# Optimization experiments

Measured on AMD Instinct MI355X. Metric: run time of the kernel, lower is better.

## Reference

```python
import jax, jax.numpy as jnp
import numpy as np

B, D, C = 4096, 256, 32000
T = 1.0
P_MARGIN = 0.5
N_MARGIN = 0.5
W_BU = 1.0
W_MS = 0.0
SIM_CAP = 0.999999


def setup_inputs() -> dict:
    key = jax.random.key(0)
    k1, k2, k3, k4, k5 = jax.random.split(key, 5)
    inputs = jax.random.normal(k1, (B, D), dtype=jnp.float32)
    inputs = inputs / jnp.linalg.norm(inputs, axis=1, keepdims=True)  # re-id features are L2-normalized
    targets = jax.random.randint(k2, (B,), 0, C, dtype=jnp.int32)
    indexs = jnp.arange(B, dtype=jnp.int32)
    label_to_pairs = jax.random.randint(k3, (B, 2), 0, B, dtype=jnp.int32)
    all_label_to_clusterid = jax.random.randint(k4, (C,), 0, C, dtype=jnp.int32)
    V = jax.random.normal(k5, (C, D), dtype=jnp.float32)
    V = V / jnp.linalg.norm(V, axis=1, keepdims=True)  # memory bank rows kept unit-norm by EMA update
    return {"inputs": inputs, "targets": targets, "indexs": indexs,
            "label_to_pairs": label_to_pairs,
            "all_label_to_clusterid": all_label_to_clusterid, "V": V}


def _ms_loss(inputs, targets):
    # vectorized form of ExLoss.ms with ms_table=False:
    # psims[i] = sims[i, targets==targets[i]], nsims[i] = sims[i, targets!=targets[i]]
    sims = inputs @ inputs.T  # [B, B]
    pos = targets[:, None] == targets[None, :]
    neg = ~pos
    NEG_BIG = jnp.float32(-1e30)
    POS_BIG = jnp.float32(1e30)
    p_thrd = jnp.where(neg.any(axis=1),
                       jnp.where(neg, sims, NEG_BIG).max(axis=1),
                       jnp.float32(-3.0)) + P_MARGIN
    n_thrd = jnp.where(pos.any(axis=1),
                       jnp.where(pos, sims, POS_BIG).min(axis=1),
                       jnp.float32(3.0)) - N_MARGIN
    hp = pos & (sims < p_thrd[:, None])
    hn = neg & (sims > n_thrd[:, None]) & (sims < SIM_CAP)
    hp_cnt = hp.sum()
    hn_cnt = hn.sum()
    # BCE-with-logits: target 1 -> softplus(-x); target 0 -> softplus(x); mean over kept elems
    hp_loss = jnp.where(hp_cnt > 0,
                        jnp.where(hp, jax.nn.softplus(-sims), 0.0).sum()
                        / jnp.maximum(hp_cnt, 1).astype(sims.dtype),
                        jnp.float32(0.0))
    hn_loss = jnp.where(hn_cnt > 0,
                        jnp.where(hn, jax.nn.softplus(sims), 0.0).sum()
                        / jnp.maximum(hn_cnt, 1).astype(sims.dtype),
                        jnp.float32(0.0))
    return hp_loss + hn_loss


def reference(inputs, targets, indexs, label_to_pairs, all_label_to_clusterid, V):
    # Exclusive.forward: logits against the memory bank
    tsims = inputs @ V.T            # [B, C]
    outputs = tsims * T
    # bu cross-entropy (weight=None, mean reduction)
    logp = jax.nn.log_softmax(outputs, axis=-1)
    bu_loss = -jnp.take_along_axis(logp, targets[:, None].astype(jnp.int32), axis=1).mean()
    ms_loss = _ms_loss(inputs, targets)
    loss = W_MS * ms_loss + W_BU * bu_loss
    return (loss, outputs)
```

## Files before the change

kernel.cpp:

```cpp
#include <hip/hip_runtime.h>
#include <hip/hip_bf16.h>
#include <stdint.h>

#define NB 4096
#define ND 256
#define NC 32000
#define NCT (NC / 128)

typedef __bf16 bf16x8 __attribute__((ext_vector_type(8)));
typedef float  f32x4  __attribute__((ext_vector_type(4)));

__device__ __forceinline__ unsigned short f32_to_bf16(float f) {
  union { float f; uint32_t u; } v; v.f = f;
  uint32_t r = v.u + 0x7fffu + ((v.u >> 16) & 1u);
  return (unsigned short)(r >> 16);
}

__global__ void prep_kernel(const float* __restrict__ inA,
                            const float* __restrict__ inV,
                            unsigned short* __restrict__ outA,
                            unsigned short* __restrict__ outV,
                            float* __restrict__ loss) {
  int gid = blockIdx.x * blockDim.x + threadIdx.x;
  int stride = gridDim.x * blockDim.x;
  if (gid == 0) *loss = 0.f;
  const int nA4 = NB * ND / 4;
  const int nV4 = NC * ND / 4;
  for (int i = gid; i < nA4 + nV4; i += stride) {
    float4 v = (i < nA4) ? ((const float4*)inA)[i]
                         : ((const float4*)inV)[i - nA4];
    ushort4 o;
    o.x = f32_to_bf16(v.x);
    o.y = f32_to_bf16(v.y);
    o.z = f32_to_bf16(v.z);
    o.w = f32_to_bf16(v.w);
    if (i < nA4) ((ushort4*)outA)[i] = o;
    else         ((ushort4*)outV)[i - nA4] = o;
  }
}

__global__ void __launch_bounds__(256, 2)
gemm_expsum_kernel(const unsigned short* __restrict__ A,
                   const unsigned short* __restrict__ V,
                   float* __restrict__ out,
                   float* __restrict__ partial) {
  __shared__ float red[2][128];

  const int b = blockIdx.x;
  const int xcd = b & 7;
  const int s = b >> 3;
  const int colt = (xcd << 5) + (s & 31);
  const int rowt = s >> 5;
  if (colt >= NCT) return;
  const int brow = rowt << 7;
  const int bcol = colt << 7;

  const int tid  = threadIdx.x;
  const int lane = tid & 63;
  const int wave = tid >> 6;
  const int wr   = wave >> 1;
  const int wc   = wave & 1;
  const int c16  = lane & 15;
  const int kq   = lane >> 4;

  const __bf16* Ab = (const __bf16*)A;
  const __bf16* Vb = (const __bf16*)V;
  const __bf16* aBase = Ab + (size_t)(brow + wr * 64 + c16) * ND + kq * 8;
  const __bf16* bBase = Vb + (size_t)(bcol + wc * 64 + c16) * ND + kq * 8;

  f32x4 acc[4][4];
#pragma unroll
  for (int c = 0; c < 4; ++c)
#pragma unroll
    for (int r = 0; r < 4; ++r)
      acc[c][r] = (f32x4){0.f, 0.f, 0.f, 0.f};

  bf16x8 a0[4], b0[4], a1[4], b1[4];

#define LOADF(AF, BF, KT)                                                     \
  do {                                                                        \
    _Pragma("unroll")                                                         \
    for (int m = 0; m < 4; ++m)                                               \
      AF[m] = *(const bf16x8*)(aBase + (size_t)m * 16 * ND + (KT) * 32);      \
    _Pragma("unroll")                                                         \
    for (int n = 0; n < 4; ++n)                                               \
      BF[n] = *(const bf16x8*)(bBase + (size_t)n * 16 * ND + (KT) * 32);      \
  } while (0)

#define MFMAALL(AF, BF)                                                       \
  do {                                                                        \
    _Pragma("unroll")                                                         \
    for (int c = 0; c < 4; ++c)                                               \
      _Pragma("unroll")                                                       \
      for (int r = 0; r < 4; ++r)                                             \
        acc[c][r] = __builtin_amdgcn_mfma_f32_16x16x32_bf16(BF[c], AF[r],     \
                                                            acc[c][r], 0, 0, 0); \
  } while (0)

  LOADF(a0, b0, 0);
#pragma unroll
  for (int kt = 0; kt < 8; kt += 2) {
    if (kt + 1 < 8) LOADF(a1, b1, kt + 1);
    MFMAALL(a0, b0);
    if (kt + 2 < 8) LOADF(a0, b0, kt + 2);
    MFMAALL(a1, b1);
  }

#pragma unroll
  for (int r = 0; r < 4; ++r) {
    const int grow = brow + wr * 64 + r * 16 + c16;
    float* prow = out + (size_t)grow * NC + (bcol + wc * 64 + kq * 4);
    float sum = 0.f;
#pragma unroll
    for (int c = 0; c < 4; ++c) {
      f32x4 v = acc[c][r];
      *(f32x4*)(prow + c * 16) = v;
      sum += __expf(v[0]) + __expf(v[1]) + __expf(v[2]) + __expf(v[3]);
    }
    sum += __shfl_xor(sum, 16);
    sum += __shfl_xor(sum, 32);
    if (lane < 16) red[wc][wr * 64 + r * 16 + c16] = sum;
  }
  __syncthreads();
  if (tid < 128)
    partial[(size_t)colt * NB + brow + tid] = red[0][tid] + red[1][tid];
#undef LOADF
#undef MFMAALL
}

__global__ void finalize_kernel(const float* __restrict__ partial,
                                const float* __restrict__ out,
                                const int* __restrict__ targets,
                                float* __restrict__ loss) {
  int r = blockIdx.x * blockDim.x + threadIdx.x;
  float s = 0.f;
  for (int c = 0; c < NCT; ++c) s += partial[(size_t)c * NB + r];
  float li = logf(s) - out[(size_t)r * NC + targets[r]];
#pragma unroll
  for (int o = 32; o > 0; o >>= 1) li += __shfl_down(li, o);
  __shared__ float wsum[4];
  int lane = threadIdx.x & 63, wv = threadIdx.x >> 6;
  if (lane == 0) wsum[wv] = li;
  __syncthreads();
  if (threadIdx.x == 0) {
    float bs = wsum[0] + wsum[1] + wsum[2] + wsum[3];
    atomicAdd(loss, bs * (1.0f / NB));
  }
}

extern "C" void kernel_launch(void* const* d_in, const int* in_sizes, int n_in,
                              void* d_out, int out_size, void* d_ws, size_t ws_size,
                              hipStream_t stream) {
  const float* inputs  = (const float*)d_in[0];
  const int*   targets = (const int*)d_in[1];
  const float* V       = (const float*)d_in[5];

  float* loss    = (float*)d_out;
  float* outputs = (float*)d_out + 1;

  char* ws = (char*)d_ws;
  unsigned short* Abf = (unsigned short*)ws;
  unsigned short* Vbf = (unsigned short*)(ws + (size_t)NB * ND * 2);
  float* partial = (float*)(ws + (size_t)NB * ND * 2 + (size_t)NC * ND * 2);

  hipLaunchKernelGGL(prep_kernel, dim3(2048), dim3(256), 0, stream,
                     inputs, V, Abf, Vbf, loss);
  hipLaunchKernelGGL(gemm_expsum_kernel, dim3(8 * 1024), dim3(256), 0, stream,
                     Abf, Vbf, outputs, partial);
  hipLaunchKernelGGL(finalize_kernel, dim3(NB / 256), dim3(256), 0, stream,
                     partial, outputs, targets, loss);
}
```

Before: 343.3 us.

## Stage GEMM tiles through swizzled LDS via direct global-to-LDS loads

Replaces the per-wave direct global fragment loads with cooperative global_load_lds staging of 128x64 A and V tiles into XOR-swizzled shared memory. Each tile is now fetched once per block instead of once per wave. Occupancy is raised to three blocks per CU, and output stores become nontemporal to avoid polluting cache with the large logits matrix. The K loop has no double buffering, so two barriers per K step serialize load and compute.

```diff
diff --git a/kernel.cpp b/kernel.cpp
--- a/kernel.cpp
+++ b/kernel.cpp
@@ -6,9 +6,15 @@
 #define ND 256
 #define NC 32000
 #define NCT (NC / 128)
+#define BK 64
 
 typedef __bf16 bf16x8 __attribute__((ext_vector_type(8)));
 typedef float  f32x4  __attribute__((ext_vector_type(4)));
+
+#define GLDS16(g, l)                                                          \
+  __builtin_amdgcn_global_load_lds(                                           \
+      (const __attribute__((address_space(1))) void*)(g),                     \
+      (__attribute__((address_space(3))) void*)(l), 16, 0, 0)
 
 __device__ __forceinline__ unsigned short f32_to_bf16(float f) {
   union { float f; uint32_t u; } v; v.f = f;
@@ -39,11 +45,13 @@
   }
 }
 
-__global__ void __launch_bounds__(256, 2)
+__global__ void __launch_bounds__(256, 3)
 gemm_expsum_kernel(const unsigned short* __restrict__ A,
                    const unsigned short* __restrict__ V,
                    float* __restrict__ out,
                    float* __restrict__ partial) {
+  __shared__ unsigned short As[128 * BK];
+  __shared__ unsigned short Vs[128 * BK];
   __shared__ float red[2][128];
 
   const int b = blockIdx.x;
@@ -63,10 +71,16 @@
   const int c16  = lane & 15;
   const int kq   = lane >> 4;
 
-  const __bf16* Ab = (const __bf16*)A;
-  const __bf16* Vb = (const __bf16*)V;
-  const __bf16* aBase = Ab + (size_t)(brow + wr * 64 + c16) * ND + kq * 8;
-  const __bf16* bBase = Vb + (size_t)(bcol + wc * 64 + c16) * ND + kq * 8;
+  const char* Ab = (const char*)A;
+  const char* Vb = (const char*)V;
+
+  int srow[4], sgrp[4];
+#pragma unroll
+  for (int i = 0; i < 4; ++i) {
+    const int chunk = i * 256 + tid;
+    srow[i] = chunk >> 3;
+    sgrp[i] = (chunk & 7) ^ (srow[i] & 7);
+  }
 
   f32x4 acc[4][4];
 #pragma unroll
@@ -75,35 +89,43 @@
     for (int r = 0; r < 4; ++r)
       acc[c][r] = (f32x4){0.f, 0.f, 0.f, 0.f};
 
-  bf16x8 a0[4], b0[4], a1[4], b1[4];
+  for (int kt = 0; kt < ND / BK; ++kt) {
+    const int kb = kt * (BK * 2);
+#pragma unroll
+    for (int i = 0; i < 4; ++i) {
+      char* ldst = (char*)As + (i * 256 + wave * 64) * 16;
+      GLDS16(Ab + (size_t)(brow + srow[i]) * 512 + kb + sgrp[i] * 16, ldst);
+    }
+#pragma unroll
+    for (int i = 0; i < 4; ++i) {
+      char* ldst = (char*)Vs + (i * 256 + wave * 64) * 16;
+      GLDS16(Vb + (size_t)(bcol + srow[i]) * 512 + kb + sgrp[i] * 16, ldst);
+    }
+    __syncthreads();
 
-#define LOADF(AF, BF, KT)                                                     \
-  do {                                                                        \
-    _Pragma("unroll")                                                         \
-    for (int m = 0; m < 4; ++m)                                               \
-      AF[m] = *(const bf16x8*)(aBase + (size_t)m * 16 * ND + (KT) * 32);      \
-    _Pragma("unroll")                                                         \
-    for (int n = 0; n < 4; ++n)                                               \
-      BF[n] = *(const bf16x8*)(bBase + (size_t)n * 16 * ND + (KT) * 32);      \
-  } while (0)
-
-#define MFMAALL(AF, BF)                                                       \
-  do {                                                                        \
-    _Pragma("unroll")                                                         \
-    for (int c = 0; c < 4; ++c)                                               \
-      _Pragma("unroll")                                                       \
-      for (int r = 0; r < 4; ++r)                                             \
-        acc[c][r] = __builtin_amdgcn_mfma_f32_16x16x32_bf16(BF[c], AF[r],     \
-                                                            acc[c][r], 0, 0, 0); \
-  } while (0)
-
-  LOADF(a0, b0, 0);
+    bf16x8 af[4][2], vf[4][2];
 #pragma unroll
-  for (int kt = 0; kt < 8; kt += 2) {
-    if (kt + 1 < 8) LOADF(a1, b1, kt + 1);
-    MFMAALL(a0, b0);
-    if (kt + 2 < 8) LOADF(a0, b0, kt + 2);
-    MFMAALL(a1, b1);
+    for (int m = 0; m < 4; ++m) {
+      const int arow = wr * 64 + m * 16 + c16;
+      const int vrow = wc * 64 + m * 16 + c16;
+#pragma unroll
+      for (int ks = 0; ks < 2; ++ks) {
+        const int g = ks * 4 + kq;
+        af[m][ks] = *(const bf16x8*)((const char*)As + arow * 128 +
+                                     ((g ^ (arow & 7)) * 16));
+        vf[m][ks] = *(const bf16x8*)((const char*)Vs + vrow * 128 +
+                                     ((g ^ (vrow & 7)) * 16));
+      }
+    }
+#pragma unroll
+    for (int ks = 0; ks < 2; ++ks)
+#pragma unroll
+      for (int c = 0; c < 4; ++c)
+#pragma unroll
+        for (int r = 0; r < 4; ++r)
+          acc[c][r] = __builtin_amdgcn_mfma_f32_16x16x32_bf16(
+              vf[c][ks], af[r][ks], acc[c][r], 0, 0, 0);
+    __syncthreads();
   }
 
 #pragma unroll
@@ -114,7 +136,7 @@
 #pragma unroll
     for (int c = 0; c < 4; ++c) {
       f32x4 v = acc[c][r];
-      *(f32x4*)(prow + c * 16) = v;
+      __builtin_nontemporal_store(v, (f32x4*)(prow + c * 16));
       sum += __expf(v[0]) + __expf(v[1]) + __expf(v[2]) + __expf(v[3]);
     }
     sum += __shfl_xor(sum, 16);
@@ -124,8 +146,6 @@
   __syncthreads();
   if (tid < 128)
     partial[(size_t)colt * NB + brow + tid] = red[0][tid] + red[1][tid];
-#undef LOADF
-#undef MFMAALL
 }
 
 __global__ void finalize_kernel(const float* __restrict__ partial,
```

Measured after the change: 398.6 us. 16.1% more time.

## Retile GEMM to 64x640 blocks with 512 threads and per-wave wide column strips

Applied to the files above, without the earlier changes.

Replaces the 128x128 block tile with a 64-row by 640-column tile, giving 50 column tiles that divide the 32000 columns exactly, so no blocks exit early. Each of 8 waves computes 16 rows by 320 columns from 20 MFMA accumulators, loading one A fragment per k-step and reusing it across 20 V fragments. The block-to-XCD mapping is changed so consecutive groups of blocks share V column strips. The double-buffered prefetch is dropped and per-lane register pressure rises, which may lower occupancy or expose global load latency. The finalize loop now sums 50 partials instead of 250.

```diff
diff --git a/kernel.cpp b/kernel.cpp
--- a/kernel.cpp
+++ b/kernel.cpp
@@ -5,7 +5,10 @@
 #define NB 4096
 #define ND 256
 #define NC 32000
-#define NCT (NC / 128)
+#define WR 64
+#define WC 640
+#define NRT (NB / WR)
+#define NCT (NC / WC)
 
 typedef __bf16 bf16x8 __attribute__((ext_vector_type(8)));
 typedef float  f32x4  __attribute__((ext_vector_type(4)));
@@ -39,93 +42,65 @@
   }
 }
 
-__global__ void __launch_bounds__(256, 2)
+__global__ void __launch_bounds__(512, 2)
 gemm_expsum_kernel(const unsigned short* __restrict__ A,
                    const unsigned short* __restrict__ V,
                    float* __restrict__ out,
                    float* __restrict__ partial) {
-  __shared__ float red[2][128];
+  __shared__ float red[2][64];
 
   const int b = blockIdx.x;
-  const int xcd = b & 7;
-  const int s = b >> 3;
-  const int colt = (xcd << 5) + (s & 31);
-  const int rowt = s >> 5;
-  if (colt >= NCT) return;
-  const int brow = rowt << 7;
-  const int bcol = colt << 7;
+  const int g = (b & 7) * (NRT * NCT / 8) + (b >> 3);
+  const int colt = g >> 6;
+  const int rowt = g & 63;
+  const int brow = rowt * WR;
+  const int bcol = colt * WC;
 
   const int tid  = threadIdx.x;
   const int lane = tid & 63;
   const int wave = tid >> 6;
-  const int wr   = wave >> 1;
-  const int wc   = wave & 1;
+  const int rf   = wave & 3;
+  const int cg   = wave >> 2;
   const int c16  = lane & 15;
   const int kq   = lane >> 4;
 
   const __bf16* Ab = (const __bf16*)A;
   const __bf16* Vb = (const __bf16*)V;
-  const __bf16* aBase = Ab + (size_t)(brow + wr * 64 + c16) * ND + kq * 8;
-  const __bf16* bBase = Vb + (size_t)(bcol + wc * 64 + c16) * ND + kq * 8;
+  const __bf16* aB = Ab + (size_t)(brow + rf * 16 + c16) * ND + kq * 8;
+  const __bf16* vB = Vb + (size_t)(bcol + cg * 320 + c16) * ND + kq * 8;
 
-  f32x4 acc[4][4];
+  f32x4 acc[20];
 #pragma unroll
-  for (int c = 0; c < 4; ++c)
+  for (int f = 0; f < 20; ++f) acc[f] = (f32x4){0.f, 0.f, 0.f, 0.f};
+
 #pragma unroll
-    for (int r = 0; r < 4; ++r)
-      acc[c][r] = (f32x4){0.f, 0.f, 0.f, 0.f};
-
-  bf16x8 a0[4], b0[4], a1[4], b1[4];
-
-#define LOADF(AF, BF, KT)                                                     \
-  do {                                                                        \
-    _Pragma("unroll")                                                         \
-    for (int m = 0; m < 4; ++m)                                               \
-      AF[m] = *(const bf16x8*)(aBase + (size_t)m * 16 * ND + (KT) * 32);      \
-    _Pragma("unroll")                                                         \
-    for (int n = 0; n < 4; ++n)                                               \
-      BF[n] = *(const bf16x8*)(bBase + (size_t)n * 16 * ND + (KT) * 32);      \
-  } while (0)
-
-#define MFMAALL(AF, BF)                                                       \
-  do {                                                                        \
-    _Pragma("unroll")                                                         \
-    for (int c = 0; c < 4; ++c)                                               \
-      _Pragma("unroll")                                                       \
-      for (int r = 0; r < 4; ++r)                                             \
-        acc[c][r] = __builtin_amdgcn_mfma_f32_16x16x32_bf16(BF[c], AF[r],     \
-                                                            acc[c][r], 0, 0, 0); \
-  } while (0)
-
-  LOADF(a0, b0, 0);
+  for (int kt = 0; kt < 8; ++kt) {
+    bf16x8 af = *(const bf16x8*)(aB + kt * 32);
+    bf16x8 vf[20];
 #pragma unroll
-  for (int kt = 0; kt < 8; kt += 2) {
-    if (kt + 1 < 8) LOADF(a1, b1, kt + 1);
-    MFMAALL(a0, b0);
-    if (kt + 2 < 8) LOADF(a0, b0, kt + 2);
-    MFMAALL(a1, b1);
+    for (int f = 0; f < 20; ++f)
+      vf[f] = *(const bf16x8*)(vB + (size_t)f * 16 * ND + kt * 32);
+#pragma unroll
+    for (int f = 0; f < 20; ++f)
+      acc[f] = __builtin_amdgcn_mfma_f32_16x16x32_bf16(vf[f], af, acc[f],
+                                                       0, 0, 0);
   }
 
+  const int grow = brow + rf * 16 + c16;
+  float* prow = out + (size_t)grow * NC + (bcol + cg * 320 + kq * 4);
+  float rsum = 0.f;
 #pragma unroll
-  for (int r = 0; r < 4; ++r) {
-    const int grow = brow + wr * 64 + r * 16 + c16;
-    float* prow = out + (size_t)grow * NC + (bcol + wc * 64 + kq * 4);
-    float sum = 0.f;
-#pragma unroll
-    for (int c = 0; c < 4; ++c) {
-      f32x4 v = acc[c][r];
-      *(f32x4*)(prow + c * 16) = v;
-      sum += __expf(v[0]) + __expf(v[1]) + __expf(v[2]) + __expf(v[3]);
-    }
-    sum += __shfl_xor(sum, 16);
-    sum += __shfl_xor(sum, 32);
-    if (lane < 16) red[wc][wr * 64 + r * 16 + c16] = sum;
+  for (int f = 0; f < 20; ++f) {
+    f32x4 v = acc[f];
+    *(f32x4*)(prow + f * 16) = v;
+    rsum += __expf(v[0]) + __expf(v[1]) + __expf(v[2]) + __expf(v[3]);
   }
+  rsum += __shfl_xor(rsum, 16);
+  rsum += __shfl_xor(rsum, 32);
+  if (lane < 16) red[cg][rf * 16 + c16] = rsum;
   __syncthreads();
-  if (tid < 128)
+  if (tid < 64)
     partial[(size_t)colt * NB + brow + tid] = red[0][tid] + red[1][tid];
-#undef LOADF
-#undef MFMAALL
 }
 
 __global__ void finalize_kernel(const float* __restrict__ partial,
@@ -134,6 +109,7 @@
                                 float* __restrict__ loss) {
   int r = blockIdx.x * blockDim.x + threadIdx.x;
   float s = 0.f;
+#pragma unroll 5
   for (int c = 0; c < NCT; ++c) s += partial[(size_t)c * NB + r];
   float li = logf(s) - out[(size_t)r * NC + targets[r]];
 #pragma unroll
@@ -165,7 +141,7 @@
 
   hipLaunchKernelGGL(prep_kernel, dim3(2048), dim3(256), 0, stream,
                      inputs, V, Abf, Vbf, loss);
-  hipLaunchKernelGGL(gemm_expsum_kernel, dim3(8 * 1024), dim3(256), 0, stream,
+  hipLaunchKernelGGL(gemm_expsum_kernel, dim3(NRT * NCT), dim3(512), 0, stream,
                      Abf, Vbf, outputs, partial);
   hipLaunchKernelGGL(finalize_kernel, dim3(NB / 256), dim3(256), 0, stream,
                      partial, outputs, targets, loss);
```

Measured after the change: 589.5 us. +71.7%, slower.
